# Kernel optimization log

Measured on AMD Instinct MI355X. Metric: run time of the kernel, lower is better.

## Reference

```python
import jax, jax.numpy as jnp
import numpy as np

D_MODEL = 2048
D_INNER = 2048
D_XB = 512
N_HEADS = 32
HEADDIM = 64   # P
DSTATE = 64    # N
N_KV = D_XB // DSTATE          # 8 kv heads
REP = N_HEADS // N_KV
D_FF = 8192
DCONV = 4
EPS = 1e-5
B, L = 1, 2048


def _rmsnorm(x, w, eps=EPS):
    return x * jax.lax.rsqrt(jnp.mean(x * x, axis=-1, keepdims=True) + eps) * w


def _silu(x):
    return x * jax.nn.sigmoid(x)


def _causal_dwconv(x, w, b):
    # x: (B,L,C), depthwise causal conv, kernel DCONV
    xp = jnp.pad(x, ((0, 0), (DCONV - 1, 0), (0, 0)))
    y = b
    for k in range(DCONV):  # small fixed kernel loop
        y = y + xp[:, k:k + x.shape[1], :] * w[:, k]
    return y


def setup_inputs() -> dict:
    key = jax.random.key(0)
    ks = jax.random.split(key, 10)
    s = 0.02
    d_proj = 2 * D_INNER + 2 * D_XB + N_HEADS  # z, x, B, C, dt
    conv_ch = 2 * D_XB + D_INNER               # conv over concat(x, B, C)
    return {
        "hidden_states": jax.random.normal(ks[0], (B, L, D_MODEL), jnp.float32),
        "in_proj_w": jax.random.normal(ks[1], (d_proj, D_MODEL), jnp.float32) * s,
        "conv_w": jax.random.normal(ks[2], (conv_ch, DCONV), jnp.float32) * s,
        "conv_b": jnp.zeros((conv_ch,), jnp.float32),
        "dt_bias": jax.random.normal(ks[3], (N_HEADS,), jnp.float32) * s,
        "A_log": jnp.log(jnp.arange(1, N_HEADS + 1, dtype=jnp.float32)),
        "D": jnp.ones((N_HEADS,), jnp.float32),
        "ssm_norm_w": jnp.ones((D_INNER,), jnp.float32),
        "out_proj_w": jax.random.normal(ks[4], (D_MODEL, D_INNER), jnp.float32) * s,
        "input_ln_w": jnp.ones((D_MODEL,), jnp.float32),
        "post_ln_w": jnp.ones((D_MODEL,), jnp.float32),
        "gate_w": jax.random.normal(ks[5], (D_FF, D_MODEL), jnp.float32) * s,
        "up_w": jax.random.normal(ks[6], (D_FF, D_MODEL), jnp.float32) * s,
        "down_w": jax.random.normal(ks[7], (D_MODEL, D_FF), jnp.float32) * s,
    }


def _mamba2(hs, in_proj_w, conv_w, conv_b, dt_bias, A_log, D, ssm_norm_w, out_proj_w):
    b, l, _ = hs.shape
    zxbcdt = hs @ in_proj_w.T
    z, x, Bm, Cm, dt = jnp.split(
        zxbcdt, [D_INNER, D_INNER + D_XB, D_INNER + 2 * D_XB, 2 * D_INNER + 2 * D_XB], axis=-1)
    # causal depthwise conv + silu over concat(x, B, C)
    xBC = _silu(_causal_dwconv(jnp.concatenate([x, Bm, Cm], axis=-1), conv_w, conv_b))
    x, Bm, Cm = jnp.split(xBC, [D_XB, 2 * D_XB], axis=-1)
    # heads (GQA: repeat x and B from N_KV to N_HEADS)
    x = jnp.repeat(x.reshape(b, l, N_KV, HEADDIM), REP, axis=2)      # (b,l,H,P)
    Bm = jnp.repeat(Bm.reshape(b, l, N_KV, DSTATE), REP, axis=2)     # (b,l,H,N)
    Cm = Cm.reshape(b, l, N_HEADS, DSTATE)                            # (b,l,H,N)
    dt = jax.nn.softplus(dt + dt_bias)                                # (b,l,H)
    dA = jnp.exp(dt * (-jnp.exp(A_log)))                              # (b,l,H)
    # selective scan over time
    xs = (jnp.moveaxis(dA, 1, 0), jnp.moveaxis(dt, 1, 0),
          jnp.moveaxis(x, 1, 0), jnp.moveaxis(Bm, 1, 0), jnp.moveaxis(Cm, 1, 0))
    h0 = jnp.zeros((b, N_HEADS, HEADDIM, DSTATE), hs.dtype)

    def step(h, t):
        dA_t, dt_t, x_t, B_t, C_t = t
        h = h * dA_t[:, :, None, None] + jnp.einsum('bh,bhp,bhn->bhpn', dt_t, x_t, B_t)
        y = jnp.einsum('bhpn,bhn->bhp', h, C_t)
        return h, y

    _, ys = jax.lax.scan(step, h0, xs)            # (l,b,H,P)
    y = jnp.moveaxis(ys, 0, 1) + D[None, None, :, None] * x
    y = y.reshape(b, l, D_INNER)
    y = _rmsnorm(y * _silu(z), ssm_norm_w)        # gated RMSNorm
    return y @ out_proj_w.T


def reference(hidden_states, in_proj_w, conv_w, conv_b, dt_bias, A_log, D,
              ssm_norm_w, out_proj_w, input_ln_w, post_ln_w, gate_w, up_w, down_w):
    residual = hidden_states
    h = _rmsnorm(hidden_states, input_ln_w)
    h = residual + _mamba2(h, in_proj_w, conv_w, conv_b, dt_bias, A_log, D,
                           ssm_norm_w, out_proj_w)
    residual = h
    h = _rmsnorm(h, post_ln_w)
    h = (_silu(h @ gate_w.T) * (h @ up_w.T)) @ down_w.T
    return residual + h
```

## Files before the change

### kernel.cpp

```cpp
#include <hip/hip_runtime.h>

typedef unsigned short u16;
typedef unsigned int u32;
typedef float f32x4 __attribute__((ext_vector_type(4)));
typedef __bf16 bf16x8 __attribute__((ext_vector_type(8)));
typedef unsigned short u16x8 __attribute__((ext_vector_type(8)));

#define L_SEQ 2048
#define DMODEL 2048
#define DINNER 2048
#define DXB 512
#define NHEADS 32
#define DPROJ 5152
#define DPROJ_PAD 5376
#define CONVCH 3072
#define DFF 8192
#define NCHUNK 32
#define CHUNK 64

__device__ __forceinline__ float bf2f(u16 u) {
  union { unsigned int i; float f; } v; v.i = ((unsigned int)u) << 16; return v.f;
}
__device__ __forceinline__ u16 f2bf(float f) {
  union { float f; unsigned int i; } v; v.f = f;
  unsigned int u = v.i;
  u += 0x7FFFu + ((u >> 16) & 1u);
  return (u16)(u >> 16);
}
__device__ __forceinline__ float siluf(float x) { return x / (1.f + __expf(-x)); }

#define GL16(gsrc, ldst) \
  __builtin_amdgcn_global_load_lds((const __attribute__((address_space(1))) u32*)(gsrc), \
                                   (__attribute__((address_space(3))) u32*)(ldst), 16, 0, 0)
#define SBAR() __builtin_amdgcn_s_barrier()
#define WAIT_VM4() asm volatile("s_waitcnt vmcnt(4)" ::: "memory")
#define WAIT_VM0() asm volatile("s_waitcnt vmcnt(0)" ::: "memory")

__global__ __launch_bounds__(256) void cvt_k(
    const float* __restrict__ s, u16* __restrict__ d, int n8)
{
  const int i = blockIdx.x * 256 + threadIdx.x;
  if (i >= n8) return;
  f32x4 a = *(const f32x4*)(s + (size_t)i * 8);
  f32x4 b = *(const f32x4*)(s + (size_t)i * 8 + 4);
  u16x8 o;
#pragma unroll
  for (int j = 0; j < 4; ++j) { o[j] = f2bf(a[j]); o[j + 4] = f2bf(b[j]); }
  *(u16x8*)(d + (size_t)i * 8) = o;
}

__global__ __launch_bounds__(256) void cvt_pad_k(
    const float* __restrict__ s, u16* __restrict__ d)
{
  const int i = blockIdx.x * 256 + threadIdx.x;
  const int row = (i * 8) >> 11;
  u16x8 o;
  if (row < DPROJ) {
    f32x4 a = *(const f32x4*)(s + (size_t)i * 8);
    f32x4 b = *(const f32x4*)(s + (size_t)i * 8 + 4);
#pragma unroll
    for (int j = 0; j < 4; ++j) { o[j] = f2bf(a[j]); o[j + 4] = f2bf(b[j]); }
  } else {
#pragma unroll
    for (int j = 0; j < 8; ++j) o[j] = 0;
  }
  *(u16x8*)(d + (size_t)i * 8) = o;
}

template<int MH, int NH>
__device__ __forceinline__ void mfma16(f32x4 (&acc)[8][4], const bf16x8 (&af)[4][2],
                                       const bf16x8 (&bfq)[2][2][2]) {
#pragma unroll
  for (int s = 0; s < 2; ++s)
#pragma unroll
    for (int m = 0; m < 4; ++m)
#pragma unroll
      for (int n = 0; n < 2; ++n)
        acc[MH * 4 + m][NH * 2 + n] = __builtin_amdgcn_mfma_f32_16x16x32_bf16(
            af[m][s], bfq[NH][n][s], acc[MH * 4 + m][NH * 2 + n], 0, 0, 0);
}

template<int EPI, int SPLIT>
__global__ __launch_bounds__(512, 2) void gemm8(
    const u16* __restrict__ A, const u16* __restrict__ W,
    void* __restrict__ Cptr, const u16* __restrict__ gateB,
    const int N, const int K, const int gx)
{
  __shared__ u16 sm[65536];
  const int tid = threadIdx.x;
  const int wid = tid >> 6, ln = tid & 63;
  const int wm = wid >> 2, wn = wid & 3;

  const int nwg = gridDim.x;
  int wg = (int)blockIdx.x;
  wg = (wg & 7) * (nwg >> 3) + (wg >> 3);
  const int tilesPerZ = gx << 3;
  const int bz = wg / tilesPerZ;
  const int rem = wg - bz * tilesPerZ;
  const int bx = rem >> 3;
  const int by = rem & 7;
  const int m0 = by << 8, n0 = bx << 8;
  const int NT = (K >> 6) / SPLIT;
  const int ktB = bz * NT;

  f32x4 acc[8][4];
#pragma unroll
  for (int i = 0; i < 8; ++i)
#pragma unroll
    for (int j = 0; j < 4; ++j) acc[i][j] = f32x4{0.f, 0.f, 0.f, 0.f};

  const int l8r = ln >> 3;
  const int schunk = (ln & 7) ^ l8r;
  const int lr16 = ln & 15;
  const int q4 = ln >> 4;
  const int swz = ln & 7;
  const int c0 = ((q4 ^ swz) << 3);

  auto stageA = [&](int buf, int kt, int h) {
#pragma unroll
    for (int g = 0; g < 2; ++g) {
      const int rr = (wid << 3) + l8r;
      const size_t grow = (size_t)(m0 + (g << 7) + (h << 6) + rr);
      const u16* src = A + grow * K + (size_t)((ktB + kt) << 6) + (schunk << 3);
      u16* dst = &sm[(buf << 15) + (((h << 7) + (g << 6) + (wid << 3)) << 6)];
      GL16(src, dst);
    }
  };
  auto stageB = [&](int buf, int kt, int h) {
#pragma unroll
    for (int g = 0; g < 2; ++g) {
      const int v = (g << 6) + (wid << 3) + l8r;
      const int grow = n0 + ((v >> 5) << 6) + (h << 5) + (v & 31);
      const u16* src = W + (size_t)grow * K + (size_t)((ktB + kt) << 6) + (schunk << 3);
      u16* dst = &sm[(buf << 15) + 16384 + (((h << 7) + (g << 6) + (wid << 3)) << 6)];
      GL16(src, dst);
    }
  };

  bf16x8 af[4][2], bfq[2][2][2];
  auto loadA = [&](int buf, int mh) {
#pragma unroll
    for (int m = 0; m < 4; ++m) {
      const int lrA = (mh << 7) + (wm << 6) + (m << 4) + lr16;
      const u16* p = &sm[(buf << 15) + (lrA << 6)];
      af[m][0] = *(const bf16x8*)(p + c0);
      af[m][1] = *(const bf16x8*)(p + (c0 ^ 32));
    }
  };
  auto loadB = [&](int buf, int nh) {
#pragma unroll
    for (int n = 0; n < 2; ++n) {
      const int lrB = (nh << 7) + (wn << 5) + (n << 4) + lr16;
      const u16* p = &sm[(buf << 15) + 16384 + (lrB << 6)];
      bfq[nh][n][0] = *(const bf16x8*)(p + c0);
      bfq[nh][n][1] = *(const bf16x8*)(p + (c0 ^ 32));
    }
  };

  stageA(0, 0, 0); stageA(0, 0, 1); stageB(0, 0, 0); stageB(0, 0, 1);
  stageA(1, 1, 0); stageB(1, 1, 1);
  WAIT_VM4();
  SBAR();

  for (int kt = 0; kt < NT; kt += 2) {
    const bool s2 = (kt + 2) < NT, s3 = (kt + 3) < NT;
    loadA(0, 0); loadB(0, 0);
    stageA(1, kt + 1, 1);
    __builtin_amdgcn_s_setprio(1); mfma16<0, 0>(acc, af, bfq); __builtin_amdgcn_s_setprio(0);
    SBAR();
    loadB(0, 1);
    stageB(1, kt + 1, 0);
    __builtin_amdgcn_s_setprio(1); mfma16<0, 1>(acc, af, bfq); __builtin_amdgcn_s_setprio(0);
    SBAR();
    loadA(0, 1);
    if (s2) stageA(0, kt + 2, 0);
    __builtin_amdgcn_s_setprio(1); mfma16<1, 1>(acc, af, bfq); __builtin_amdgcn_s_setprio(0);
    SBAR();
    if (s2) stageB(0, kt + 2, 1);
    __builtin_amdgcn_s_setprio(1); mfma16<1, 0>(acc, af, bfq); __builtin_amdgcn_s_setprio(0);
    if (s2) { WAIT_VM4(); } else { WAIT_VM0(); }
    SBAR();
    loadA(1, 0); loadB(1, 0);
    if (s2) stageA(0, kt + 2, 1);
    __builtin_amdgcn_s_setprio(1); mfma16<0, 0>(acc, af, bfq); __builtin_amdgcn_s_setprio(0);
    SBAR();
    loadB(1, 1);
    if (s2) stageB(0, kt + 2, 0);
    __builtin_amdgcn_s_setprio(1); mfma16<0, 1>(acc, af, bfq); __builtin_amdgcn_s_setprio(0);
    SBAR();
    loadA(1, 1);
    if (s3) stageA(1, kt + 3, 0);
    __builtin_amdgcn_s_setprio(1); mfma16<1, 1>(acc, af, bfq); __builtin_amdgcn_s_setprio(0);
    SBAR();
    if (s3) stageB(1, kt + 3, 1);
    __builtin_amdgcn_s_setprio(1); mfma16<1, 0>(acc, af, bfq); __builtin_amdgcn_s_setprio(0);
    if (s2) { if (s3) { WAIT_VM4(); } else { WAIT_VM0(); } }
    SBAR();
  }

  const int crow0 = m0 + (wm << 7) + (q4 << 2);
  const int ccol0 = n0 + (wn << 6) + lr16;
#pragma unroll
  for (int M = 0; M < 8; ++M) {
#pragma unroll
    for (int n = 0; n < 4; ++n) {
      const int col = ccol0 + (n << 4);
      if (col < N) {
#pragma unroll
        for (int j = 0; j < 4; ++j) {
          const size_t idx = (size_t)(crow0 + (M << 4) + j) * N + col;
          if (EPI == 0) {
            ((u16*)Cptr)[idx] = f2bf(acc[M][n][j]);
          } else if (EPI == 2) {
            float* P = (float*)Cptr + (size_t)bz * ((size_t)L_SEQ * N);
            P[idx] = acc[M][n][j];
          } else {
            ((u16*)Cptr)[idx] = f2bf(siluf(bf2f(gateB[idx])) * acc[M][n][j]);
          }
        }
      }
    }
  }
}

__global__ __launch_bounds__(256) void rmsnorm_k(
    const float* __restrict__ in, const float* __restrict__ w, u16* __restrict__ out)
{
  const int row = blockIdx.x, tid = threadIdx.x;
  const float* r = in + (size_t)row * DMODEL + tid * 8;
  f32x4 v0 = *(const f32x4*)r;
  f32x4 v1 = *(const f32x4*)(r + 4);
  float ss = v0[0]*v0[0] + v0[1]*v0[1] + v0[2]*v0[2] + v0[3]*v0[3]
           + v1[0]*v1[0] + v1[1]*v1[1] + v1[2]*v1[2] + v1[3]*v1[3];
#pragma unroll
  for (int off = 1; off < 64; off <<= 1) ss += __shfl_xor(ss, off);
  __shared__ float part[4];
  if ((tid & 63) == 0) part[tid >> 6] = ss;
  __syncthreads();
  const float tot = part[0] + part[1] + part[2] + part[3];
  const float scale = rsqrtf(tot * (1.f / DMODEL) + 1e-5f);
  f32x4 w0 = *(const f32x4*)(w + tid * 8);
  f32x4 w1 = *(const f32x4*)(w + tid * 8 + 4);
  u16x8 o;
#pragma unroll
  for (int j = 0; j < 4; ++j) {
    o[j]     = f2bf(v0[j] * scale * w0[j]);
    o[j + 4] = f2bf(v1[j] * scale * w1[j]);
  }
  *(u16x8*)(out + (size_t)row * DMODEL + tid * 8) = o;
}

__global__ __launch_bounds__(256) void red4_rms_k(
    const float* __restrict__ P, const float* __restrict__ resid,
    float* __restrict__ hres, const float* __restrict__ w, u16* __restrict__ h2)
{
  const int row = blockIdx.x, tid = threadIdx.x;
  const size_t base = (size_t)row * DMODEL + tid * 8;
  const size_t stride = (size_t)L_SEQ * DMODEL;
  f32x4 v0 = *(const f32x4*)(resid + base);
  f32x4 v1 = *(const f32x4*)(resid + base + 4);
#pragma unroll
  for (int p = 0; p < 4; ++p) {
    v0 += *(const f32x4*)(P + p * stride + base);
    v1 += *(const f32x4*)(P + p * stride + base + 4);
  }
  *(f32x4*)(hres + base) = v0;
  *(f32x4*)(hres + base + 4) = v1;
  float ss = v0[0]*v0[0] + v0[1]*v0[1] + v0[2]*v0[2] + v0[3]*v0[3]
           + v1[0]*v1[0] + v1[1]*v1[1] + v1[2]*v1[2] + v1[3]*v1[3];
#pragma unroll
  for (int off = 1; off < 64; off <<= 1) ss += __shfl_xor(ss, off);
  __shared__ float part[4];
  if ((tid & 63) == 0) part[tid >> 6] = ss;
  __syncthreads();
  const float tot = part[0] + part[1] + part[2] + part[3];
  const float scale = rsqrtf(tot * (1.f / DMODEL) + 1e-5f);
  f32x4 w0 = *(const f32x4*)(w + tid * 8);
  f32x4 w1 = *(const f32x4*)(w + tid * 8 + 4);
  u16x8 o;
#pragma unroll
  for (int j = 0; j < 4; ++j) {
    o[j]     = f2bf(v0[j] * scale * w0[j]);
    o[j + 4] = f2bf(v1[j] * scale * w1[j]);
  }
  *(u16x8*)(h2 + base) = o;
}

__global__ __launch_bounds__(256) void red4_add_k(
    const float* __restrict__ P, const float* __restrict__ resid, float* __restrict__ out)
{
  const size_t base = ((size_t)blockIdx.x * 256 + threadIdx.x) * 8;
  const size_t stride = (size_t)L_SEQ * DMODEL;
  f32x4 v0 = *(const f32x4*)(resid + base);
  f32x4 v1 = *(const f32x4*)(resid + base + 4);
#pragma unroll
  for (int p = 0; p < 4; ++p) {
    v0 += *(const f32x4*)(P + p * stride + base);
    v1 += *(const f32x4*)(P + p * stride + base + 4);
  }
  *(f32x4*)(out + base) = v0;
  *(f32x4*)(out + base + 4) = v1;
}

__global__ __launch_bounds__(256) void gated_rms_k(
    const float* __restrict__ y, const u16* __restrict__ zx,
    const float* __restrict__ w, u16* __restrict__ out)
{
  const int row = blockIdx.x, tid = threadIdx.x;
  const float* yr = y + (size_t)row * DINNER + tid * 8;
  f32x4 y0 = *(const f32x4*)yr;
  f32x4 y1 = *(const f32x4*)(yr + 4);
  u16x8 zv = *(const u16x8*)(zx + (size_t)row * DPROJ + tid * 8);
  float val[8];
#pragma unroll
  for (int j = 0; j < 4; ++j) {
    val[j]     = y0[j] * siluf(bf2f(zv[j]));
    val[j + 4] = y1[j] * siluf(bf2f(zv[j + 4]));
  }
  float ss = 0.f;
#pragma unroll
  for (int j = 0; j < 8; ++j) ss += val[j] * val[j];
#pragma unroll
  for (int off = 1; off < 64; off <<= 1) ss += __shfl_xor(ss, off);
  __shared__ float part[4];
  if ((tid & 63) == 0) part[tid >> 6] = ss;
  __syncthreads();
  const float tot = part[0] + part[1] + part[2] + part[3];
  const float scale = rsqrtf(tot * (1.f / DINNER) + 1e-5f);
  u16x8 o;
#pragma unroll
  for (int j = 0; j < 8; ++j) o[j] = f2bf(val[j] * scale * w[tid * 8 + j]);
  *(u16x8*)(out + (size_t)row * DINNER + tid * 8) = o;
}

__global__ __launch_bounds__(256) void convdt_k(
    const u16* __restrict__ zx, const float* __restrict__ w,
    const float* __restrict__ b, u16* __restrict__ xbc,
    const float* __restrict__ dt_bias, const float* __restrict__ A_log,
    float* __restrict__ dtv, float* __restrict__ dAv)
{
  if (blockIdx.x < 3072) {
    const int flat = blockIdx.x * 256 + threadIdx.x;
    const int t = flat / 384;
    const int c8 = (flat % 384) * 8;
    float acc[8];
    f32x4 b0 = *(const f32x4*)(b + c8);
    f32x4 b1 = *(const f32x4*)(b + c8 + 4);
#pragma unroll
    for (int j = 0; j < 4; ++j) { acc[j] = b0[j]; acc[j + 4] = b1[j]; }
    f32x4 wr[8];
#pragma unroll
    for (int j = 0; j < 8; ++j) wr[j] = *(const f32x4*)(w + (size_t)(c8 + j) * 4);
#pragma unroll
    for (int k = 0; k < 4; ++k) {
      const int tt = t - 3 + k;
      if (tt >= 0) {
        u16x8 xv = *(const u16x8*)(zx + (size_t)tt * DPROJ + DINNER + c8);
#pragma unroll
        for (int j = 0; j < 8; ++j) acc[j] += bf2f(xv[j]) * wr[j][k];
      }
    }
    u16x8 o;
#pragma unroll
    for (int j = 0; j < 8; ++j) o[j] = f2bf(siluf(acc[j]));
    *(u16x8*)(xbc + (size_t)t * CONVCH + c8) = o;
  } else {
    const int flat = (blockIdx.x - 3072) * 256 + threadIdx.x;
    const int t = flat >> 5, h = flat & 31;
    const float x = bf2f(zx[(size_t)t * DPROJ + (DPROJ - NHEADS) + h]) + dt_bias[h];
    const float sp = (x > 20.f) ? x : log1pf(expf(x));
    const float a = expf(A_log[h]);
    dtv[flat] = sp;
    dAv[flat] = expf(-a * sp);
  }
}

__device__ __forceinline__ void stage16(float* dst, const u16* src) {
  u16x8 a = *(const u16x8*)src;
  u16x8 b = *(const u16x8*)(src + 8);
#pragma unroll
  for (int j = 0; j < 8; ++j) { dst[j] = bf2f(a[j]); dst[8 + j] = bf2f(b[j]); }
}

__global__ __launch_bounds__(256) void scan_a(
    const u16* __restrict__ xbc, const float* __restrict__ dtv,
    const float* __restrict__ dAv, const float* __restrict__ Dvec,
    float* __restrict__ y, float* __restrict__ S,
    float* __restrict__ gam, float* __restrict__ cum)
{
  __shared__ float xs[64][64], Bs[64][64], Cs[64][64];
  __shared__ float dts[64], dAs[64];
  const int c = blockIdx.x, h = blockIdx.y, kv = h >> 2;
  const int tid = threadIdx.x;
  const int t0 = c * CHUNK;
  {
    const int r = tid >> 2, cq = (tid & 3) * 16;
    const u16* base = xbc + (size_t)(t0 + r) * CONVCH;
    stage16(&xs[r][cq], base + kv * 64 + cq);
    stage16(&Bs[r][cq], base + DXB + kv * 64 + cq);
    stage16(&Cs[r][cq], base + 2 * DXB + h * 64 + cq);
    if (tid < 64) {
      dts[tid] = dtv[(size_t)(t0 + tid) * NHEADS + h];
      dAs[tid] = dAv[(size_t)(t0 + tid) * NHEADS + h];
    }
  }
  __syncthreads();
  const int p = tid >> 2, q = tid & 3;
  float hreg[16];
#pragma unroll
  for (int i = 0; i < 16; ++i) hreg[i] = 0.f;
  float cumv = 1.f;
  const float Dh = Dvec[h];
  for (int t = 0; t < CHUNK; ++t) {
    const float dtt = dts[t], dat = dAs[t];
    const float xv = xs[t][p];
    const float u = dtt * xv;
    float a0 = 0.f, a1 = 0.f, a2 = 0.f, a3 = 0.f;
#pragma unroll
    for (int i4 = 0; i4 < 4; ++i4) {
      f32x4 b4 = *(const f32x4*)&Bs[t][q * 16 + i4 * 4];
      f32x4 c4 = *(const f32x4*)&Cs[t][q * 16 + i4 * 4];
#pragma unroll
      for (int j = 0; j < 4; ++j) {
        const int i = i4 * 4 + j;
        hreg[i] = hreg[i] * dat + u * b4[j];
        if (i4 == 0) a0 += hreg[i] * c4[j];
        else if (i4 == 1) a1 += hreg[i] * c4[j];
        else if (i4 == 2) a2 += hreg[i] * c4[j];
        else a3 += hreg[i] * c4[j];
      }
    }
    float accv = (a0 + a1) + (a2 + a3);
    accv += __shfl_xor(accv, 1);
    accv += __shfl_xor(accv, 2);
    cumv *= dat;
    if (q == 0) y[(size_t)(t0 + t) * DINNER + h * 64 + p] = accv + Dh * xv;
    if (tid == 0) cum[(size_t)(t0 + t) * NHEADS + h] = cumv;
  }
  float* Sp = S + ((size_t)(c * NHEADS + h) << 12) + tid * 16;
#pragma unroll
  for (int i4 = 0; i4 < 4; ++i4)
    *(f32x4*)(Sp + i4 * 4) = f32x4{hreg[i4*4], hreg[i4*4+1], hreg[i4*4+2], hreg[i4*4+3]};
  if (tid == 0) gam[c * NHEADS + h] = cumv;
}

__global__ __launch_bounds__(256) void scan_b(
    const float* __restrict__ S, const float* __restrict__ gam, float* __restrict__ H)
{
  const int g = blockIdx.x * 256 + threadIdx.x;
  const int h = g >> 12;
  const int e = g & 4095;
  float hr = 0.f;
  for (int c = 0; c < NCHUNK; ++c) {
    const size_t base = (((size_t)(c * NHEADS + h)) << 12) + e;
    H[base] = hr;
    hr = gam[c * NHEADS + h] * hr + S[base];
  }
}

__global__ __launch_bounds__(256) void scan_c(
    const u16* __restrict__ xbc, const float* __restrict__ cum,
    const float* __restrict__ H, float* __restrict__ y)
{
  __shared__ float Cs[64][64];
  __shared__ float cums[64];
  const int c = blockIdx.x, h = blockIdx.y, tid = threadIdx.x;
  const int t0 = c * CHUNK;
  {
    const int r = tid >> 2, cq = (tid & 3) * 16;
    stage16(&Cs[r][cq], xbc + (size_t)(t0 + r) * CONVCH + 2 * DXB + h * 64 + cq);
    if (tid < 64) cums[tid] = cum[(size_t)(t0 + tid) * NHEADS + h];
  }
  const int p = tid >> 2, q = tid & 3;
  float hr[16];
  const size_t base = ((size_t)(c * NHEADS + h) << 12) + tid * 16;
#pragma unroll
  for (int i4 = 0; i4 < 4; ++i4) {
    f32x4 v = *(const f32x4*)(H + base + i4 * 4);
#pragma unroll
    for (int j = 0; j < 4; ++j) hr[i4 * 4 + j] = v[j];
  }
  __syncthreads();
  for (int t = 0; t < CHUNK; ++t) {
    float accv = 0.f;
#pragma unroll
    for (int i4 = 0; i4 < 4; ++i4) {
      f32x4 c4 = *(const f32x4*)&Cs[t][q * 16 + i4 * 4];
#pragma unroll
      for (int j = 0; j < 4; ++j) accv += hr[i4 * 4 + j] * c4[j];
    }
    accv += __shfl_xor(accv, 1);
    accv += __shfl_xor(accv, 2);
    if (q == 0) {
      const size_t idx = (size_t)(t0 + t) * DINNER + h * 64 + p;
      y[idx] += cums[t] * accv;
    }
  }
}

extern "C" void kernel_launch(void* const* d_in, const int* in_sizes, int n_in,
                              void* d_out, int out_size, void* d_ws, size_t ws_size,
                              hipStream_t stream) {
  const float* hs         = (const float*)d_in[0];
  const float* in_proj_w  = (const float*)d_in[1];
  const float* conv_w     = (const float*)d_in[2];
  const float* conv_b     = (const float*)d_in[3];
  const float* dt_bias    = (const float*)d_in[4];
  const float* A_log      = (const float*)d_in[5];
  const float* Dv         = (const float*)d_in[6];
  const float* ssm_w      = (const float*)d_in[7];
  const float* out_proj_w = (const float*)d_in[8];
  const float* in_ln_w    = (const float*)d_in[9];
  const float* post_ln_w  = (const float*)d_in[10];
  const float* gate_w     = (const float*)d_in[11];
  const float* up_w       = (const float*)d_in[12];
  const float* down_w     = (const float*)d_in[13];
  float* out = (float*)d_out;

  char* ws = (char*)d_ws;
  size_t off = 0;
  auto alloc = [&](size_t bytes) -> void* {
    void* p = ws + off;
    off = (off + bytes + 255) & ~(size_t)255;
    return p;
  };
  u16* wip = (u16*)alloc((size_t)DPROJ_PAD * DMODEL * 2);
  u16* wop = (u16*)alloc((size_t)DMODEL * DINNER * 2);
  u16* wg  = (u16*)alloc((size_t)DFF    * DMODEL * 2);
  u16* wu  = (u16*)alloc((size_t)DFF    * DMODEL * 2);
  u16* wd  = (u16*)alloc((size_t)DMODEL * DFF    * 2);
  u16*   zx  = (u16*)  alloc((size_t)L_SEQ * DPROJ * 2);
  u16*   xbc = (u16*)  alloc((size_t)L_SEQ * CONVCH * 2);
  float* Sv  = (float*)alloc((size_t)NCHUNK * NHEADS * 4096 * 4);
  float* Hv  = (float*)alloc((size_t)NCHUNK * NHEADS * 4096 * 4);
  float* pK  = (float*)zx;
  float* dtv = (float*)alloc((size_t)L_SEQ * NHEADS * 4);
  float* dAv = (float*)alloc((size_t)L_SEQ * NHEADS * 4);
  float* cum = (float*)alloc((size_t)L_SEQ * NHEADS * 4);
  float* gam = (float*)alloc((size_t)NCHUNK * NHEADS * 4);
  float* yv  = (float*)alloc((size_t)L_SEQ * DINNER * 4);
  float* hres= (float*)alloc((size_t)L_SEQ * DMODEL * 4);
  u16*  gateb= (u16*)  alloc((size_t)L_SEQ * DFF * 2);
  u16*  hslot= (u16*)  alloc((size_t)L_SEQ * DMODEL * 2);
  (void)ws_size; (void)in_sizes; (void)n_in; (void)out_size;

  cvt_pad_k<<<(DPROJ_PAD * DMODEL / 8) / 256, 256, 0, stream>>>(in_proj_w, wip);
  cvt_k<<<DMODEL * DINNER / 8 / 256, 256, 0, stream>>>(out_proj_w, wop, DMODEL * DINNER / 8);
  cvt_k<<<DFF * DMODEL / 8 / 256, 256, 0, stream>>>(gate_w, wg, DFF * DMODEL / 8);
  cvt_k<<<DFF * DMODEL / 8 / 256, 256, 0, stream>>>(up_w, wu, DFF * DMODEL / 8);
  cvt_k<<<DMODEL * DFF / 8 / 256, 256, 0, stream>>>(down_w, wd, DMODEL * DFF / 8);

  rmsnorm_k<<<L_SEQ, 256, 0, stream>>>(hs, in_ln_w, hslot);
  gemm8<0, 1><<<21 * 8, 512, 0, stream>>>(hslot, wip, zx, nullptr, DPROJ, DMODEL, 21);
  convdt_k<<<3072 + 256, 256, 0, stream>>>(zx, conv_w, conv_b, xbc, dt_bias, A_log, dtv, dAv);
  scan_a<<<dim3(NCHUNK, NHEADS), 256, 0, stream>>>(xbc, dtv, dAv, Dv, yv, Sv, gam, cum);
  scan_b<<<512, 256, 0, stream>>>(Sv, gam, Hv);
  scan_c<<<dim3(NCHUNK, NHEADS), 256, 0, stream>>>(xbc, cum, Hv, yv);
  gated_rms_k<<<L_SEQ, 256, 0, stream>>>(yv, zx, ssm_w, hslot);
  gemm8<2, 4><<<8 * 8 * 4, 512, 0, stream>>>(hslot, wop, pK, nullptr, DMODEL, DINNER, 8);
  red4_rms_k<<<L_SEQ, 256, 0, stream>>>(pK, hs, hres, post_ln_w, hslot);
  gemm8<0, 1><<<32 * 8, 512, 0, stream>>>(hslot, wg, gateb, nullptr, DFF, DMODEL, 32);
  gemm8<3, 1><<<32 * 8, 512, 0, stream>>>(hslot, wu, gateb, gateb, DFF, DMODEL, 32);
  gemm8<2, 4><<<8 * 8 * 4, 512, 0, stream>>>(gateb, wd, pK, nullptr, DMODEL, DFF, 8);
  red4_add_k<<<(L_SEQ * DMODEL / 8) / 256, 256, 0, stream>>>(pK, hres, out);
}
```

Baseline: 501.5 us.

## Store split-K partials as bf16 and split the in_proj GEMM two ways

The split-K GEMM epilogue now writes bf16 partials instead of fp32, and the reduction kernels read bf16 and accumulate in fp32. This halves the partial-sum traffic for out_proj and down_proj. The in_proj GEMM becomes a 2-way split-K launch with twice as many blocks, followed by a new kernel that sums the two partials into the zx buffer. The partials reuse the xbc workspace and spill into later scratch buffers. The cost is extra rounding in the bf16 partials and one more kernel launch plus a round trip through memory for in_proj.

```diff
diff --git a/kernel.cpp b/kernel.cpp
--- a/kernel.cpp
+++ b/kernel.cpp
@@ -212,8 +212,8 @@
           if (EPI == 0) {
             ((u16*)Cptr)[idx] = f2bf(acc[M][n][j]);
           } else if (EPI == 2) {
-            float* P = (float*)Cptr + (size_t)bz * ((size_t)L_SEQ * N);
-            P[idx] = acc[M][n][j];
+            u16* P = (u16*)Cptr + (size_t)bz * ((size_t)L_SEQ * N);
+            P[idx] = f2bf(acc[M][n][j]);
           } else {
             ((u16*)Cptr)[idx] = f2bf(siluf(bf2f(gateB[idx])) * acc[M][n][j]);
           }
@@ -250,8 +250,21 @@
   *(u16x8*)(out + (size_t)row * DMODEL + tid * 8) = o;
 }
 
+__global__ __launch_bounds__(256) void red2bf_k(
+    const u16* __restrict__ P, u16* __restrict__ out)
+{
+  const size_t i = ((size_t)blockIdx.x * 256 + threadIdx.x) * 8;
+  const size_t stride = (size_t)L_SEQ * DPROJ;
+  u16x8 a = *(const u16x8*)(P + i);
+  u16x8 b = *(const u16x8*)(P + stride + i);
+  u16x8 o;
+#pragma unroll
+  for (int j = 0; j < 8; ++j) o[j] = f2bf(bf2f(a[j]) + bf2f(b[j]));
+  *(u16x8*)(out + i) = o;
+}
+
 __global__ __launch_bounds__(256) void red4_rms_k(
-    const float* __restrict__ P, const float* __restrict__ resid,
+    const u16* __restrict__ P, const float* __restrict__ resid,
     float* __restrict__ hres, const float* __restrict__ w, u16* __restrict__ h2)
 {
   const int row = blockIdx.x, tid = threadIdx.x;
@@ -261,8 +274,9 @@
   f32x4 v1 = *(const f32x4*)(resid + base + 4);
 #pragma unroll
   for (int p = 0; p < 4; ++p) {
-    v0 += *(const f32x4*)(P + p * stride + base);
-    v1 += *(const f32x4*)(P + p * stride + base + 4);
+    u16x8 pv = *(const u16x8*)(P + p * stride + base);
+#pragma unroll
+    for (int j = 0; j < 4; ++j) { v0[j] += bf2f(pv[j]); v1[j] += bf2f(pv[j + 4]); }
   }
   *(f32x4*)(hres + base) = v0;
   *(f32x4*)(hres + base + 4) = v1;
@@ -287,7 +301,7 @@
 }
 
 __global__ __launch_bounds__(256) void red4_add_k(
-    const float* __restrict__ P, const float* __restrict__ resid, float* __restrict__ out)
+    const u16* __restrict__ P, const float* __restrict__ resid, float* __restrict__ out)
 {
   const size_t base = ((size_t)blockIdx.x * 256 + threadIdx.x) * 8;
   const size_t stride = (size_t)L_SEQ * DMODEL;
@@ -295,8 +309,9 @@
   f32x4 v1 = *(const f32x4*)(resid + base + 4);
 #pragma unroll
   for (int p = 0; p < 4; ++p) {
-    v0 += *(const f32x4*)(P + p * stride + base);
-    v1 += *(const f32x4*)(P + p * stride + base + 4);
+    u16x8 pv = *(const u16x8*)(P + p * stride + base);
+#pragma unroll
+    for (int j = 0; j < 4; ++j) { v0[j] += bf2f(pv[j]); v1[j] += bf2f(pv[j + 4]); }
   }
   *(f32x4*)(out + base) = v0;
   *(f32x4*)(out + base + 4) = v1;
@@ -533,7 +548,8 @@
   u16*   xbc = (u16*)  alloc((size_t)L_SEQ * CONVCH * 2);
   float* Sv  = (float*)alloc((size_t)NCHUNK * NHEADS * 4096 * 4);
   float* Hv  = (float*)alloc((size_t)NCHUNK * NHEADS * 4096 * 4);
-  float* pK  = (float*)zx;
+  u16*   pIn = xbc;
+  u16*   pK  = zx;
   float* dtv = (float*)alloc((size_t)L_SEQ * NHEADS * 4);
   float* dAv = (float*)alloc((size_t)L_SEQ * NHEADS * 4);
   float* cum = (float*)alloc((size_t)L_SEQ * NHEADS * 4);
@@ -551,7 +567,8 @@
   cvt_k<<<DMODEL * DFF / 8 / 256, 256, 0, stream>>>(down_w, wd, DMODEL * DFF / 8);
 
   rmsnorm_k<<<L_SEQ, 256, 0, stream>>>(hs, in_ln_w, hslot);
-  gemm8<0, 1><<<21 * 8, 512, 0, stream>>>(hslot, wip, zx, nullptr, DPROJ, DMODEL, 21);
+  gemm8<2, 2><<<21 * 8 * 2, 512, 0, stream>>>(hslot, wip, pIn, nullptr, DPROJ, DMODEL, 21);
+  red2bf_k<<<(L_SEQ * DPROJ / 8) / 256, 256, 0, stream>>>(pIn, zx);
   convdt_k<<<3072 + 256, 256, 0, stream>>>(zx, conv_w, conv_b, xbc, dt_bias, A_log, dtv, dAv);
   scan_a<<<dim3(NCHUNK, NHEADS), 256, 0, stream>>>(xbc, dtv, dAv, Dv, yv, Sv, gam, cum);
   scan_b<<<512, 256, 0, stream>>>(Sv, gam, Hv);
```

After: 511.3 us. About the same (+2.0%).
